# Optimization experiments

Hardware: AMD Instinct MI355X
Metric: run time of the kernel (lower is better)

## Reference

```python
import jax, jax.numpy as jnp
from jax import lax
import numpy as np

N_HEADS, N_FEATURES, IMG_W, IMG_H, C_DOWN = 8, 64, 96, 96, 32


def setup_inputs() -> dict:
    key = jax.random.key(0)
    ks = jax.random.split(key, 16)
    d = {
        'X': jax.random.normal(ks[0], (N_FEATURES, IMG_W, IMG_H), jnp.float32),
        'WQ_task': jax.random.normal(ks[1], (N_HEADS, N_FEATURES, 1, 1), jnp.float32),
        'BQ_task': jax.random.normal(ks[2], (N_HEADS, N_FEATURES, 1, 1), jnp.float32),
        'WK_task': jax.random.normal(ks[3], (N_FEATURES, 1, 1), jnp.float32),
        'BK_task': jax.random.normal(ks[4], (N_FEATURES, 1, 1), jnp.float32),
        'WV_task': jax.random.normal(ks[5], (1, C_DOWN, 1, 1), jnp.float32),
        'BV_task': jax.random.normal(ks[6], (1, C_DOWN, 1, 1), jnp.float32),
        # learned parameters (loaded from disk in the original)
        'WQ_t_minus_1': jax.random.uniform(ks[7], (N_HEADS, N_FEATURES, 1, 1), jnp.float32),
        'WQ_x': jax.random.uniform(ks[8], (1, N_FEATURES, 1, 1), jnp.float32),
        'BQ': jax.random.uniform(ks[9], (N_HEADS, N_FEATURES, 1, 1), jnp.float32),
        'WK_x': jax.random.uniform(ks[10], (N_FEATURES, 1, 1), jnp.float32),
        'BK': jax.random.uniform(ks[11], (N_FEATURES, 1, 1), jnp.float32),
        'Vconv_w': jax.random.normal(ks[12], (C_DOWN, N_FEATURES, 3, 3), jnp.float32) * 0.05,
        'Vconv_b': jax.random.normal(ks[13], (C_DOWN,), jnp.float32) * 0.05,
        # recurrent state (zeros at t=0 in original; random here to exercise the path)
        'prev_Q': jax.random.normal(ks[14], (N_HEADS, N_FEATURES, IMG_W, IMG_H), jnp.float32),
    }
    return d


def reference(X, WQ_task, BQ_task, WK_task, BK_task, WV_task, BV_task,
              WQ_t_minus_1, WQ_x, BQ, WK_x, BK, Vconv_w, Vconv_b, prev_Q):
    F, W, H = X.shape
    rx = X[None]  # (1, F, W, H)
    # Q: (A, F, W, H);  K: (F, W, H)
    Q = WQ_task * jax.nn.relu(WQ_t_minus_1 * prev_Q + WQ_x * rx + BQ) + BQ_task
    K = WK_task * jax.nn.relu(WK_x * X + BK) + BK_task
    # similarity[w,h,u,v] = sum_{a,f} Q[a,f,w,h] * K[f,u,v]
    #                     = sum_f (sum_a Q)[f,w,h] * K[f,u,v]  -> a (WH,F)@(F,WH) GEMM
    Qs = Q.sum(axis=0)  # (F, W, H)
    sim = jnp.einsum('fwh,fuv->whuv', Qs, K)  # (W, H, W, H)
    attn = jax.nn.softmax(sim.reshape(W, H, W * H), axis=-1)  # (W, H, WH)
    # V = task-modulated 3x3 conv of X
    Vc = lax.conv_general_dilated(rx, Vconv_w, window_strides=(1, 1), padding='SAME',
                                  dimension_numbers=('NCHW', 'OIHW', 'NCHW'))
    Vc = Vc + Vconv_b[None, :, None, None]
    V = (WV_task * Vc + BV_task)[0].reshape(C_DOWN, W * H)  # (C, WH)
    # out[c,w,h] = sum_k attn[w,h,k] * V[c,k]
    out = jnp.einsum('whk,ck->cwh', attn, V)  # (C, W, H)
    return out
```

## Files before the change

kernel.cpp:

```cpp
#include <hip/hip_runtime.h>

#define WH 9216
#define NF 64
#define NC 32
#define NH 8
#define IMGW 96
#define IMGH 96
#define PW 98
#define PPLANE 9604
#define L2E 1.4426950408889634f
#define DEFER 11.5f
#define SKIP 18.0f

typedef float f32x4 __attribute__((ext_vector_type(4)));
typedef short short8 __attribute__((ext_vector_type(8)));

__device__ inline short bf16_bits(float x) {
  __bf16 h = (__bf16)x;
  return __builtin_bit_cast(short, h);
}
__device__ inline float bf16_round(float x) { return (float)(__bf16)x; }

__global__ __launch_bounds__(256) void pad_wpack_kernel(
    const float* __restrict__ X, const float* __restrict__ Wc,
    const float* __restrict__ WV_task,
    unsigned short* __restrict__ padXT, short8* __restrict__ wfrag)
{
  const int bid = blockIdx.x;
  const int t = threadIdx.x;
  if (bid < 301) {
    const int idx = bid * 256 + t;
    if (idx < 76832) {
      const int fi = idx / PPLANE;
      const int p = idx - fi * PPLANE;
      const int pw = p / PW;
      const int ph = p - pw * PW;
      short8 r;
      if (pw >= 1 && pw <= IMGW && ph >= 1 && ph <= IMGH) {
        const float* src = X + (size_t)fi * 8 * WH + (pw - 1) * IMGH + (ph - 1);
        #pragma unroll
        for (int e = 0; e < 8; ++e) r[e] = bf16_bits(src[(size_t)e * WH]);
      } else {
        #pragma unroll
        for (int e = 0; e < 8; ++e) r[e] = 0;
      }
      *(short8*)&padXT[(size_t)p * 64 + fi * 8] = r;
    }
  } else {
    #pragma unroll
    for (int j = 0; j < 9; ++j) {
      const int ridx = j * 256 + t;
      const int ct = ridx / 1152;
      const int rem = ridx - ct * 1152;
      const int cc = rem >> 6;
      const int lane = rem & 63;
      const int c = ct * 16 + (lane & 15);
      const int tap = cc >> 1;
      const int f0 = (cc & 1) * 32 + 8 * (lane >> 4);
      const float wv = WV_task[c];
      short8 r;
      #pragma unroll
      for (int e = 0; e < 8; ++e)
        r[e] = bf16_bits(wv * Wc[((size_t)c * NF + f0 + e) * 9 + tap]);
      wfrag[ridx] = r;
    }
  }
}

__global__ __launch_bounds__(128, 2) void qsk_kernel(
    const float* __restrict__ X, const float* __restrict__ WQ_task,
    const float* __restrict__ BQ_task, const float* __restrict__ WK_task,
    const float* __restrict__ BK_task, const float* __restrict__ WQ_t1,
    const float* __restrict__ WQ_x, const float* __restrict__ BQ,
    const float* __restrict__ WK_x, const float* __restrict__ BK,
    const float* __restrict__ prevQ,
    short* __restrict__ qfrag, short* __restrict__ kfrag)
{
  const int t = threadIdx.x;
  const int lane = t & 63;
  const int fh = t >> 6;
  const int h = lane >> 4;
  const int b = blockIdx.x;
  const int T = b >> 1, sub = b & 1;
  const int wh = T * 16 + (lane & 15);
  const int f0 = fh * 32 + 8 * h + 4 * sub;

  float x[4];
  #pragma unroll
  for (int e = 0; e < 4; ++e) x[e] = X[(size_t)(f0 + e) * WH + wh];
  float pq[32];
  #pragma unroll
  for (int a = 0; a < NH; ++a)
    #pragma unroll
    for (int e = 0; e < 4; ++e)
      pq[a * 4 + e] = prevQ[(size_t)(a * 64 + f0 + e) * WH + wh];

  const float4 wkx = *(const float4*)&WK_x[f0];
  const float4 bk  = *(const float4*)&BK[f0];
  const float4 wkt = *(const float4*)&WK_task[f0];
  const float4 bkt = *(const float4*)&BK_task[f0];
  const float4 wqx = *(const float4*)&WQ_x[f0];

  float q[4], k[4], xq[4];
  k[0] = fmaf(wkt.x, fmaxf(fmaf(wkx.x, x[0], bk.x), 0.f), bkt.x);
  k[1] = fmaf(wkt.y, fmaxf(fmaf(wkx.y, x[1], bk.y), 0.f), bkt.y);
  k[2] = fmaf(wkt.z, fmaxf(fmaf(wkx.z, x[2], bk.z), 0.f), bkt.z);
  k[3] = fmaf(wkt.w, fmaxf(fmaf(wkx.w, x[3], bk.w), 0.f), bkt.w);
  xq[0] = wqx.x * x[0]; xq[1] = wqx.y * x[1];
  xq[2] = wqx.z * x[2]; xq[3] = wqx.w * x[3];
  q[0] = q[1] = q[2] = q[3] = 0.f;
  #pragma unroll
  for (int a = 0; a < NH; ++a) {
    const int af0 = a * 64 + f0;
    const float4 w1  = *(const float4*)&WQ_t1[af0];
    const float4 bq  = *(const float4*)&BQ[af0];
    const float4 wqt = *(const float4*)&WQ_task[af0];
    const float4 bqt = *(const float4*)&BQ_task[af0];
    q[0] = fmaf(wqt.x, fmaxf(fmaf(w1.x, pq[a * 4 + 0], xq[0] + bq.x), 0.f), q[0]) + bqt.x;
    q[1] = fmaf(wqt.y, fmaxf(fmaf(w1.y, pq[a * 4 + 1], xq[1] + bq.y), 0.f), q[1]) + bqt.y;
    q[2] = fmaf(wqt.z, fmaxf(fmaf(w1.z, pq[a * 4 + 2], xq[2] + bq.z), 0.f), q[2]) + bqt.z;
    q[3] = fmaf(wqt.w, fmaxf(fmaf(w1.w, pq[a * 4 + 3], xq[3] + bq.w), 0.f), q[3]) + bqt.w;
  }

  short4 qh, ql, kh, klo;
  {
    float qs0 = q[0] * L2E, qs1 = q[1] * L2E, qs2 = q[2] * L2E, qs3 = q[3] * L2E;
    qh.x = bf16_bits(qs0); ql.x = bf16_bits(qs0 - bf16_round(qs0));
    qh.y = bf16_bits(qs1); ql.y = bf16_bits(qs1 - bf16_round(qs1));
    qh.z = bf16_bits(qs2); ql.z = bf16_bits(qs2 - bf16_round(qs2));
    qh.w = bf16_bits(qs3); ql.w = bf16_bits(qs3 - bf16_round(qs3));
    kh.x = bf16_bits(k[0]); klo.x = bf16_bits(k[0] - bf16_round(k[0]));
    kh.y = bf16_bits(k[1]); klo.y = bf16_bits(k[1] - bf16_round(k[1]));
    kh.z = bf16_bits(k[2]); klo.z = bf16_bits(k[2] - bf16_round(k[2]));
    kh.w = bf16_bits(k[3]); klo.w = bf16_bits(k[3] - bf16_round(k[3]));
  }
  const size_t offh = ((size_t)(T * 4 + fh) * 64 + lane) * 8 + sub * 4;
  const size_t offl = ((size_t)(T * 4 + 2 + fh) * 64 + lane) * 8 + sub * 4;
  *(short4*)&qfrag[offh] = qh;
  *(short4*)&qfrag[offl] = ql;
  *(short4*)&kfrag[offh] = kh;
  *(short4*)&kfrag[offl] = klo;
}

__global__ __launch_bounds__(256, 1) void vconv_kernel(
    const unsigned short* __restrict__ padXT, const short8* __restrict__ wfrag,
    const float* __restrict__ bc, const float* __restrict__ WV_task,
    const float* __restrict__ BV_task, short8* __restrict__ vfrag)
{
  __shared__ float Vt[2][32][36];
  const int t = threadIdx.x;
  const int lane = t & 63, w = t >> 6;
  const int h = lane >> 4;
  const int b = blockIdx.x;
  const int ktloc = w >> 1, half = w & 1;
  const int key = (b * 2 + ktloc) * 16 + (lane & 15);
  const int kw = key / IMGH, kh = key - kw * IMGH;

  f32x4 acc0 = {0.f, 0.f, 0.f, 0.f}, acc1 = {0.f, 0.f, 0.f, 0.f};
  #pragma unroll
  for (int i = 0; i < 9; ++i) {
    const int cc = half * 9 + i;
    const int tap = cc >> 1;
    const int di = tap / 3, dj = tap - di * 3;
    const int f0 = (cc & 1) * 32 + 8 * h;
    const int sp = (kw + di) * PW + (kh + dj);
    const short8 xf = *(const short8*)&padXT[(size_t)sp * 64 + f0];
    acc0 = __builtin_amdgcn_mfma_f32_16x16x32_bf16(wfrag[(size_t)cc * 64 + lane], xf, acc0, 0, 0, 0);
    acc1 = __builtin_amdgcn_mfma_f32_16x16x32_bf16(wfrag[(size_t)(18 + cc) * 64 + lane], xf, acc1, 0, 0, 0);
  }
  const int klc = ktloc * 16 + (lane & 15);
  #pragma unroll
  for (int reg = 0; reg < 4; ++reg) {
    Vt[half][4 * h + reg][klc] = acc0[reg];
    Vt[half][16 + 4 * h + reg][klc] = acc1[reg];
  }
  __syncthreads();
  if (t < 128) {
    const int ct = t >> 6;
    const int c = ct * 16 + (lane & 15);
    const float bias = fmaf(WV_task[c], bc[c], BV_task[c]);
    short8 r;
    #pragma unroll
    for (int e = 0; e < 8; ++e) {
      const int kl2 = 16 * (e >> 2) + 4 * h + (e & 3);
      r[e] = bf16_bits(Vt[0][c][kl2] + Vt[1][c][kl2] + bias);
    }
    vfrag[((size_t)b * 2 + ct) * 64 + lane] = r;
  }
}

__global__ __launch_bounds__(256, 3) void flash_mfma(
    const short8* __restrict__ qfrag, const short8* __restrict__ kfrag,
    const short8* __restrict__ vfrag, float* __restrict__ part, int cps)
{
  const int t = threadIdx.x;
  const int lane = t & 63, wave = t >> 6;
  const int h = lane >> 4;
  const int qb = blockIdx.x;
  const int s = blockIdx.y;

  short8 qf[3][4];
  #pragma unroll
  for (int g = 0; g < 3; ++g)
    #pragma unroll
    for (int tm = 0; tm < 4; ++tm)
      qf[g][tm] = qfrag[((size_t)(qb * 3 + g) * 4 + tm) * 64 + lane];

  f32x4 acc[2][3];
  #pragma unroll
  for (int ct = 0; ct < 2; ++ct)
    #pragma unroll
    for (int g = 0; g < 3; ++g)
      acc[ct][g] = (f32x4){0.f, 0.f, 0.f, 0.f};
  float m[3] = {-1e30f, -1e30f, -1e30f};
  float l[3] = {0.f, 0.f, 0.f};

  auto softmax_pv = [&](int g, const f32x4& st0, const f32x4& st1, float tmax,
                        const short8& vf0, const short8& vf1) {
    if (__any(tmax > m[g] + DEFER)) {
      const float nm = fmaxf(m[g], tmax);
      const float r = exp2f(m[g] - nm);
      l[g] *= r;
      acc[0][g] *= r;
      acc[1][g] *= r;
      m[g] = nm;
    }
    short8 pb;
    float ls = 0.f;
    #pragma unroll
    for (int e = 0; e < 4; ++e) {
      const float p0 = exp2f(st0[e] - m[g]);
      const float p1 = exp2f(st1[e] - m[g]);
      ls += p0 + p1;
      pb[e] = bf16_bits(p0);
      pb[4 + e] = bf16_bits(p1);
    }
    l[g] += ls;
    acc[0][g] = __builtin_amdgcn_mfma_f32_16x16x32_bf16(vf0, pb, acc[0][g], 0, 0, 0);
    acc[1][g] = __builtin_amdgcn_mfma_f32_16x16x32_bf16(vf1, pb, acc[1][g], 0, 0, 0);
  };

  const int cpw = cps >> 2;
  const int ch0 = s * cps + wave;

  for (int it = 0; it < cpw; it += 8) {
    const int ch = ch0 + it * 4;
    short8 kf[2][4];
    #pragma unroll
    for (int kt = 0; kt < 2; ++kt)
      #pragma unroll
      for (int tm = 0; tm < 4; ++tm)
        kf[kt][tm] = kfrag[((size_t)(2 * ch + kt) * 4 + tm) * 64 + lane];
    const short8 vf0 = vfrag[(size_t)(ch * 2 + 0) * 64 + lane];
    const short8 vf1 = vfrag[(size_t)(ch * 2 + 1) * 64 + lane];

    #pragma unroll
    for (int g = 0; g < 3; ++g) {
      f32x4 st[2];
      #pragma unroll
      for (int kt = 0; kt < 2; ++kt) {
        f32x4 a = (f32x4){0.f, 0.f, 0.f, 0.f};
        a = __builtin_amdgcn_mfma_f32_16x16x32_bf16(kf[kt][0], qf[g][0], a, 0, 0, 0);
        a = __builtin_amdgcn_mfma_f32_16x16x32_bf16(kf[kt][1], qf[g][1], a, 0, 0, 0);
        a = __builtin_amdgcn_mfma_f32_16x16x32_bf16(kf[kt][2], qf[g][0], a, 0, 0, 0);
        a = __builtin_amdgcn_mfma_f32_16x16x32_bf16(kf[kt][3], qf[g][1], a, 0, 0, 0);
        a = __builtin_amdgcn_mfma_f32_16x16x32_bf16(kf[kt][0], qf[g][2], a, 0, 0, 0);
        a = __builtin_amdgcn_mfma_f32_16x16x32_bf16(kf[kt][1], qf[g][3], a, 0, 0, 0);
        st[kt] = a;
      }
      float tmax = -1e30f;
      #pragma unroll
      for (int e = 0; e < 4; ++e)
        tmax = fmaxf(tmax, fmaxf(st[0][e], st[1][e]));
      tmax = fmaxf(tmax, __shfl_xor(tmax, 16));
      tmax = fmaxf(tmax, __shfl_xor(tmax, 32));
      softmax_pv(g, st[0], st[1], tmax, vf0, vf1);
    }
  }

  for (int it = 0; it < cpw; ++it) {
    if ((it & 7) == 0) continue;
    const int ch = ch0 + it * 4;
    short8 kfh[2][2];
    #pragma unroll
    for (int kt = 0; kt < 2; ++kt)
      #pragma unroll
      for (int tm = 0; tm < 2; ++tm)
        kfh[kt][tm] = kfrag[((size_t)(2 * ch + kt) * 4 + tm) * 64 + lane];

    f32x4 st[2][3];
    #pragma unroll
    for (int kt = 0; kt < 2; ++kt)
      #pragma unroll
      for (int g = 0; g < 3; ++g) {
        f32x4 a = (f32x4){0.f, 0.f, 0.f, 0.f};
        a = __builtin_amdgcn_mfma_f32_16x16x32_bf16(kfh[kt][0], qf[g][0], a, 0, 0, 0);
        a = __builtin_amdgcn_mfma_f32_16x16x32_bf16(kfh[kt][1], qf[g][1], a, 0, 0, 0);
        st[kt][g] = a;
      }

    float tmax[3];
    int fire = 0;
    #pragma unroll
    for (int g = 0; g < 3; ++g) {
      float tm8 = -1e30f;
      #pragma unroll
      for (int e = 0; e < 4; ++e)
        tm8 = fmaxf(tm8, fmaxf(st[0][g][e], st[1][g][e]));
      tm8 = fmaxf(tm8, __shfl_xor(tm8, 16));
      tm8 = fmaxf(tm8, __shfl_xor(tm8, 32));
      tmax[g] = tm8;
      if (__any(tm8 > m[g] - SKIP)) fire |= 1 << g;
    }
    if (!fire) continue;

    short8 kfl[2][2];
    #pragma unroll
    for (int kt = 0; kt < 2; ++kt)
      #pragma unroll
      for (int tm = 0; tm < 2; ++tm)
        kfl[kt][tm] = kfrag[((size_t)(2 * ch + kt) * 4 + 2 + tm) * 64 + lane];
    const short8 vf0 = vfrag[(size_t)(ch * 2 + 0) * 64 + lane];
    const short8 vf1 = vfrag[(size_t)(ch * 2 + 1) * 64 + lane];

    #pragma unroll
    for (int g = 0; g < 3; ++g) {
      if (!(fire & (1 << g))) continue;
      #pragma unroll
      for (int kt = 0; kt < 2; ++kt) {
        f32x4 a = st[kt][g];
        a = __builtin_amdgcn_mfma_f32_16x16x32_bf16(kfl[kt][0], qf[g][0], a, 0, 0, 0);
        a = __builtin_amdgcn_mfma_f32_16x16x32_bf16(kfl[kt][1], qf[g][1], a, 0, 0, 0);
        a = __builtin_amdgcn_mfma_f32_16x16x32_bf16(kfh[kt][0], qf[g][2], a, 0, 0, 0);
        a = __builtin_amdgcn_mfma_f32_16x16x32_bf16(kfh[kt][1], qf[g][3], a, 0, 0, 0);
        st[kt][g] = a;
      }
      softmax_pv(g, st[0][g], st[1][g], tmax[g], vf0, vf1);
    }
  }

  const int u = s * 4 + wave;
  #pragma unroll
  for (int g = 0; g < 3; ++g) {
    float lf = l[g] + __shfl_xor(l[g], 16);
    lf += __shfl_xor(lf, 32);
    const int q = qb * 48 + g * 16 + (lane & 15);
    float* base = part + ((size_t)u * WH + q) * 36;
    *(f32x4*)(base + 0 + 4 * h) = acc[0][g];
    *(f32x4*)(base + 16 + 4 * h) = acc[1][g];
    if (h == 0) { base[32] = m[g]; base[33] = lf; }
  }
}

__global__ __launch_bounds__(256) void merge_kernel(
    const float* __restrict__ part, float* __restrict__ out, int units)
{
  const int t = threadIdx.x;
  const int cl = t & 31;
  const int wh = blockIdx.x * 8 + (t >> 5);
  float M = -1e30f;
  for (int u = 0; u < units; ++u)
    M = fmaxf(M, part[((size_t)u * WH + wh) * 36 + 32]);
  float L = 0.f, A = 0.f;
  for (int u = 0; u < units; ++u) {
    const float* base = part + ((size_t)u * WH + wh) * 36;
    const float e = exp2f(base[32] - M);
    L = fmaf(e, base[33], L);
    A = fmaf(e, base[cl], A);
  }
  out[(size_t)cl * WH + wh] = A / L;
}

extern "C" void kernel_launch(void* const* d_in, const int* in_sizes, int n_in,
                              void* d_out, int out_size, void* d_ws, size_t ws_size,
                              hipStream_t stream)
{
  const float* X   = (const float*)d_in[0];
  const float* WQt = (const float*)d_in[1];
  const float* BQt = (const float*)d_in[2];
  const float* WKt = (const float*)d_in[3];
  const float* BKt = (const float*)d_in[4];
  const float* WVt = (const float*)d_in[5];
  const float* BVt = (const float*)d_in[6];
  const float* WQ1 = (const float*)d_in[7];
  const float* WQx = (const float*)d_in[8];
  const float* BQ  = (const float*)d_in[9];
  const float* WKx = (const float*)d_in[10];
  const float* BK  = (const float*)d_in[11];
  const float* Wc  = (const float*)d_in[12];
  const float* bc  = (const float*)d_in[13];
  const float* pQ  = (const float*)d_in[14];
  float* out = (float*)d_out;

  short8* qfrag = (short8*)d_ws;
  short8* kfrag = qfrag + (size_t)147456;
  short8* vfrag = kfrag + (size_t)147456;
  short8* wfrag = vfrag + (size_t)36864;
  unsigned short* padXT = (unsigned short*)(wfrag + 2304);
  float* part = (float*)((char*)padXT + (size_t)PPLANE * 64 * 2);
  const size_t base_bytes = ((size_t)147456 * 2 + 36864 + 2304) * 16 + (size_t)PPLANE * 64 * 2;

  int ksplit = 4;
  while (ksplit > 1 &&
         base_bytes + (size_t)(4 * ksplit) * WH * 36 * sizeof(float) > ws_size)
    ksplit >>= 1;
  const int cps = 288 / ksplit;
  const int units = 4 * ksplit;

  pad_wpack_kernel<<<dim3(302), 256, 0, stream>>>(X, Wc, WVt, padXT, wfrag);
  qsk_kernel<<<dim3(1152), 128, 0, stream>>>(X, WQt, BQt, WKt, BKt,
                                             WQ1, WQx, BQ, WKx, BK, pQ,
                                             (short*)qfrag, (short*)kfrag);
  vconv_kernel<<<dim3(288), 256, 0, stream>>>(padXT, wfrag, bc, WVt, BVt, vfrag);
  flash_mfma<<<dim3(192, ksplit), 256, 0, stream>>>(qfrag, kfrag, vfrag, part, cps);
  merge_kernel<<<dim3(WH / 8), 256, 0, stream>>>(part, out, units);
}
```

Measured before the change: 91.40 us.

## Fuse prep kernels, drop chunk skipping, shrink flash tiles, online merge

Merges the Q/K projection kernel into the padding/weight-pack kernel, so there is one fewer launch. The attention kernel drops the two-pass scheme that estimated scores with high-bf16 K and skipped chunks far below the running max. It now computes full scores for every chunk, seeds the accumulator with the negated running max, and rescales only past a threshold. Each block handles 32 queries instead of 48, giving a bigger grid with higher occupancy and swapped grid axes. The vconv kernel is split into smaller per-tile blocks, and the merge becomes a single-pass online rescale. This removes skip overhead and improves parallelism, but does all the score and PV work that was previously skipped.

```diff
diff --git a/kernel.cpp b/kernel.cpp
--- a/kernel.cpp
+++ b/kernel.cpp
@@ -10,7 +10,6 @@
 #define PPLANE 9604
 #define L2E 1.4426950408889634f
 #define DEFER 11.5f
-#define SKIP 18.0f
 
 typedef float f32x4 __attribute__((ext_vector_type(4)));
 typedef short short8 __attribute__((ext_vector_type(8)));
@@ -21,15 +20,85 @@
 }
 __device__ inline float bf16_round(float x) { return (float)(__bf16)x; }
 
-__global__ __launch_bounds__(256) void pad_wpack_kernel(
-    const float* __restrict__ X, const float* __restrict__ Wc,
+__global__ __launch_bounds__(256, 2) void prep_kernel(
+    const float* __restrict__ X, const float* __restrict__ WQ_task,
+    const float* __restrict__ BQ_task, const float* __restrict__ WK_task,
+    const float* __restrict__ BK_task, const float* __restrict__ WQ_t1,
+    const float* __restrict__ WQ_x, const float* __restrict__ BQ,
+    const float* __restrict__ WK_x, const float* __restrict__ BK,
+    const float* __restrict__ prevQ, const float* __restrict__ Wc,
     const float* __restrict__ WV_task,
+    short* __restrict__ qfrag, short* __restrict__ kfrag,
     unsigned short* __restrict__ padXT, short8* __restrict__ wfrag)
 {
   const int bid = blockIdx.x;
   const int t = threadIdx.x;
-  if (bid < 301) {
-    const int idx = bid * 256 + t;
+  if (bid < 576) {
+    const int lane = t & 63;
+    const int w2 = t >> 6;
+    const int fh = w2 & 1, sub = w2 >> 1;
+    const int h = lane >> 4;
+    const int T = bid;
+    const int wh = T * 16 + (lane & 15);
+    const int f0 = fh * 32 + 8 * h + 4 * sub;
+
+    float x[4];
+    #pragma unroll
+    for (int e = 0; e < 4; ++e) x[e] = X[(size_t)(f0 + e) * WH + wh];
+    float pq[32];
+    #pragma unroll
+    for (int a = 0; a < NH; ++a)
+      #pragma unroll
+      for (int e = 0; e < 4; ++e)
+        pq[a * 4 + e] = prevQ[(size_t)(a * 64 + f0 + e) * WH + wh];
+
+    const float4 wkx = *(const float4*)&WK_x[f0];
+    const float4 bk  = *(const float4*)&BK[f0];
+    const float4 wkt = *(const float4*)&WK_task[f0];
+    const float4 bkt = *(const float4*)&BK_task[f0];
+    const float4 wqx = *(const float4*)&WQ_x[f0];
+
+    float q[4], k[4], xq[4];
+    k[0] = fmaf(wkt.x, fmaxf(fmaf(wkx.x, x[0], bk.x), 0.f), bkt.x);
+    k[1] = fmaf(wkt.y, fmaxf(fmaf(wkx.y, x[1], bk.y), 0.f), bkt.y);
+    k[2] = fmaf(wkt.z, fmaxf(fmaf(wkx.z, x[2], bk.z), 0.f), bkt.z);
+    k[3] = fmaf(wkt.w, fmaxf(fmaf(wkx.w, x[3], bk.w), 0.f), bkt.w);
+    xq[0] = wqx.x * x[0]; xq[1] = wqx.y * x[1];
+    xq[2] = wqx.z * x[2]; xq[3] = wqx.w * x[3];
+    q[0] = q[1] = q[2] = q[3] = 0.f;
+    #pragma unroll
+    for (int a = 0; a < NH; ++a) {
+      const int af0 = a * 64 + f0;
+      const float4 w1  = *(const float4*)&WQ_t1[af0];
+      const float4 bq  = *(const float4*)&BQ[af0];
+      const float4 wqt = *(const float4*)&WQ_task[af0];
+      const float4 bqt = *(const float4*)&BQ_task[af0];
+      q[0] = fmaf(wqt.x, fmaxf(fmaf(w1.x, pq[a * 4 + 0], xq[0] + bq.x), 0.f), q[0]) + bqt.x;
+      q[1] = fmaf(wqt.y, fmaxf(fmaf(w1.y, pq[a * 4 + 1], xq[1] + bq.y), 0.f), q[1]) + bqt.y;
+      q[2] = fmaf(wqt.z, fmaxf(fmaf(w1.z, pq[a * 4 + 2], xq[2] + bq.z), 0.f), q[2]) + bqt.z;
+      q[3] = fmaf(wqt.w, fmaxf(fmaf(w1.w, pq[a * 4 + 3], xq[3] + bq.w), 0.f), q[3]) + bqt.w;
+    }
+
+    short4 qh, ql, kh, klo;
+    {
+      float qs0 = q[0] * L2E, qs1 = q[1] * L2E, qs2 = q[2] * L2E, qs3 = q[3] * L2E;
+      qh.x = bf16_bits(qs0); ql.x = bf16_bits(qs0 - bf16_round(qs0));
+      qh.y = bf16_bits(qs1); ql.y = bf16_bits(qs1 - bf16_round(qs1));
+      qh.z = bf16_bits(qs2); ql.z = bf16_bits(qs2 - bf16_round(qs2));
+      qh.w = bf16_bits(qs3); ql.w = bf16_bits(qs3 - bf16_round(qs3));
+      kh.x = bf16_bits(k[0]); klo.x = bf16_bits(k[0] - bf16_round(k[0]));
+      kh.y = bf16_bits(k[1]); klo.y = bf16_bits(k[1] - bf16_round(k[1]));
+      kh.z = bf16_bits(k[2]); klo.z = bf16_bits(k[2] - bf16_round(k[2]));
+      kh.w = bf16_bits(k[3]); klo.w = bf16_bits(k[3] - bf16_round(k[3]));
+    }
+    const size_t offh = ((size_t)(T * 4 + fh) * 64 + lane) * 8 + sub * 4;
+    const size_t offl = ((size_t)(T * 4 + 2 + fh) * 64 + lane) * 8 + sub * 4;
+    *(short4*)&qfrag[offh] = qh;
+    *(short4*)&qfrag[offl] = ql;
+    *(short4*)&kfrag[offh] = kh;
+    *(short4*)&kfrag[offl] = klo;
+  } else if (bid < 877) {
+    const int idx = (bid - 576) * 256 + t;
     if (idx < 76832) {
       const int fi = idx / PPLANE;
       const int p = idx - fi * PPLANE;
@@ -67,96 +136,21 @@
   }
 }
 
-__global__ __launch_bounds__(128, 2) void qsk_kernel(
-    const float* __restrict__ X, const float* __restrict__ WQ_task,
-    const float* __restrict__ BQ_task, const float* __restrict__ WK_task,
-    const float* __restrict__ BK_task, const float* __restrict__ WQ_t1,
-    const float* __restrict__ WQ_x, const float* __restrict__ BQ,
-    const float* __restrict__ WK_x, const float* __restrict__ BK,
-    const float* __restrict__ prevQ,
-    short* __restrict__ qfrag, short* __restrict__ kfrag)
-{
-  const int t = threadIdx.x;
-  const int lane = t & 63;
-  const int fh = t >> 6;
-  const int h = lane >> 4;
-  const int b = blockIdx.x;
-  const int T = b >> 1, sub = b & 1;
-  const int wh = T * 16 + (lane & 15);
-  const int f0 = fh * 32 + 8 * h + 4 * sub;
-
-  float x[4];
-  #pragma unroll
-  for (int e = 0; e < 4; ++e) x[e] = X[(size_t)(f0 + e) * WH + wh];
-  float pq[32];
-  #pragma unroll
-  for (int a = 0; a < NH; ++a)
-    #pragma unroll
-    for (int e = 0; e < 4; ++e)
-      pq[a * 4 + e] = prevQ[(size_t)(a * 64 + f0 + e) * WH + wh];
-
-  const float4 wkx = *(const float4*)&WK_x[f0];
-  const float4 bk  = *(const float4*)&BK[f0];
-  const float4 wkt = *(const float4*)&WK_task[f0];
-  const float4 bkt = *(const float4*)&BK_task[f0];
-  const float4 wqx = *(const float4*)&WQ_x[f0];
-
-  float q[4], k[4], xq[4];
-  k[0] = fmaf(wkt.x, fmaxf(fmaf(wkx.x, x[0], bk.x), 0.f), bkt.x);
-  k[1] = fmaf(wkt.y, fmaxf(fmaf(wkx.y, x[1], bk.y), 0.f), bkt.y);
-  k[2] = fmaf(wkt.z, fmaxf(fmaf(wkx.z, x[2], bk.z), 0.f), bkt.z);
-  k[3] = fmaf(wkt.w, fmaxf(fmaf(wkx.w, x[3], bk.w), 0.f), bkt.w);
-  xq[0] = wqx.x * x[0]; xq[1] = wqx.y * x[1];
-  xq[2] = wqx.z * x[2]; xq[3] = wqx.w * x[3];
-  q[0] = q[1] = q[2] = q[3] = 0.f;
-  #pragma unroll
-  for (int a = 0; a < NH; ++a) {
-    const int af0 = a * 64 + f0;
-    const float4 w1  = *(const float4*)&WQ_t1[af0];
-    const float4 bq  = *(const float4*)&BQ[af0];
-    const float4 wqt = *(const float4*)&WQ_task[af0];
-    const float4 bqt = *(const float4*)&BQ_task[af0];
-    q[0] = fmaf(wqt.x, fmaxf(fmaf(w1.x, pq[a * 4 + 0], xq[0] + bq.x), 0.f), q[0]) + bqt.x;
-    q[1] = fmaf(wqt.y, fmaxf(fmaf(w1.y, pq[a * 4 + 1], xq[1] + bq.y), 0.f), q[1]) + bqt.y;
-    q[2] = fmaf(wqt.z, fmaxf(fmaf(w1.z, pq[a * 4 + 2], xq[2] + bq.z), 0.f), q[2]) + bqt.z;
-    q[3] = fmaf(wqt.w, fmaxf(fmaf(w1.w, pq[a * 4 + 3], xq[3] + bq.w), 0.f), q[3]) + bqt.w;
-  }
-
-  short4 qh, ql, kh, klo;
-  {
-    float qs0 = q[0] * L2E, qs1 = q[1] * L2E, qs2 = q[2] * L2E, qs3 = q[3] * L2E;
-    qh.x = bf16_bits(qs0); ql.x = bf16_bits(qs0 - bf16_round(qs0));
-    qh.y = bf16_bits(qs1); ql.y = bf16_bits(qs1 - bf16_round(qs1));
-    qh.z = bf16_bits(qs2); ql.z = bf16_bits(qs2 - bf16_round(qs2));
-    qh.w = bf16_bits(qs3); ql.w = bf16_bits(qs3 - bf16_round(qs3));
-    kh.x = bf16_bits(k[0]); klo.x = bf16_bits(k[0] - bf16_round(k[0]));
-    kh.y = bf16_bits(k[1]); klo.y = bf16_bits(k[1] - bf16_round(k[1]));
-    kh.z = bf16_bits(k[2]); klo.z = bf16_bits(k[2] - bf16_round(k[2]));
-    kh.w = bf16_bits(k[3]); klo.w = bf16_bits(k[3] - bf16_round(k[3]));
-  }
-  const size_t offh = ((size_t)(T * 4 + fh) * 64 + lane) * 8 + sub * 4;
-  const size_t offl = ((size_t)(T * 4 + 2 + fh) * 64 + lane) * 8 + sub * 4;
-  *(short4*)&qfrag[offh] = qh;
-  *(short4*)&qfrag[offl] = ql;
-  *(short4*)&kfrag[offh] = kh;
-  *(short4*)&kfrag[offl] = klo;
-}
-
-__global__ __launch_bounds__(256, 1) void vconv_kernel(
+__global__ __launch_bounds__(256, 2) void vconv_kernel(
     const unsigned short* __restrict__ padXT, const short8* __restrict__ wfrag,
     const float* __restrict__ bc, const float* __restrict__ WV_task,
-    const float* __restrict__ BV_task, short8* __restrict__ vfrag)
-{
-  __shared__ float Vt[2][32][36];
+    const float* __restrict__ BV_task, short* __restrict__ vfrag)
+{
+  __shared__ float Vt[2][32][20];
   const int t = threadIdx.x;
   const int lane = t & 63, w = t >> 6;
   const int h = lane >> 4;
-  const int b = blockIdx.x;
-  const int ktloc = w >> 1, half = w & 1;
-  const int key = (b * 2 + ktloc) * 16 + (lane & 15);
+  const int ktile = blockIdx.x;
+  const int half = w & 1, ct = w >> 1;
+  const int key = ktile * 16 + (lane & 15);
   const int kw = key / IMGH, kh = key - kw * IMGH;
 
-  f32x4 acc0 = {0.f, 0.f, 0.f, 0.f}, acc1 = {0.f, 0.f, 0.f, 0.f};
+  f32x4 acc = {0.f, 0.f, 0.f, 0.f};
   #pragma unroll
   for (int i = 0; i < 9; ++i) {
     const int cc = half * 9 + i;
@@ -165,85 +159,57 @@
     const int f0 = (cc & 1) * 32 + 8 * h;
     const int sp = (kw + di) * PW + (kh + dj);
     const short8 xf = *(const short8*)&padXT[(size_t)sp * 64 + f0];
-    acc0 = __builtin_amdgcn_mfma_f32_16x16x32_bf16(wfrag[(size_t)cc * 64 + lane], xf, acc0, 0, 0, 0);
-    acc1 = __builtin_amdgcn_mfma_f32_16x16x32_bf16(wfrag[(size_t)(18 + cc) * 64 + lane], xf, acc1, 0, 0, 0);
-  }
-  const int klc = ktloc * 16 + (lane & 15);
-  #pragma unroll
-  for (int reg = 0; reg < 4; ++reg) {
-    Vt[half][4 * h + reg][klc] = acc0[reg];
-    Vt[half][16 + 4 * h + reg][klc] = acc1[reg];
-  }
+    acc = __builtin_amdgcn_mfma_f32_16x16x32_bf16(wfrag[(size_t)(ct * 18 + cc) * 64 + lane],
+                                                  xf, acc, 0, 0, 0);
+  }
+  #pragma unroll
+  for (int reg = 0; reg < 4; ++reg)
+    Vt[half][ct * 16 + 4 * h + reg][lane & 15] = acc[reg];
   __syncthreads();
   if (t < 128) {
-    const int ct = t >> 6;
-    const int c = ct * 16 + (lane & 15);
+    const int ct2 = t >> 6;
+    const int c = ct2 * 16 + (lane & 15);
     const float bias = fmaf(WV_task[c], bc[c], BV_task[c]);
-    short8 r;
-    #pragma unroll
-    for (int e = 0; e < 8; ++e) {
-      const int kl2 = 16 * (e >> 2) + 4 * h + (e & 3);
-      r[e] = bf16_bits(Vt[0][c][kl2] + Vt[1][c][kl2] + bias);
-    }
-    vfrag[((size_t)b * 2 + ct) * 64 + lane] = r;
-  }
-}
-
-__global__ __launch_bounds__(256, 3) void flash_mfma(
+    short4 r;
+    #pragma unroll
+    for (int j = 0; j < 4; ++j) {
+      const int kl = 4 * h + j;
+      r[j] = bf16_bits(Vt[0][c][kl] + Vt[1][c][kl] + bias);
+    }
+    const int ch = ktile >> 1, eh = ktile & 1;
+    *(short4*)&vfrag[(((size_t)ch * 2 + ct2) * 64 + lane) * 8 + eh * 4] = r;
+  }
+}
+
+__global__ __launch_bounds__(256, 4) void flash_mfma(
     const short8* __restrict__ qfrag, const short8* __restrict__ kfrag,
     const short8* __restrict__ vfrag, float* __restrict__ part, int cps)
 {
   const int t = threadIdx.x;
   const int lane = t & 63, wave = t >> 6;
   const int h = lane >> 4;
-  const int qb = blockIdx.x;
-  const int s = blockIdx.y;
-
-  short8 qf[3][4];
-  #pragma unroll
-  for (int g = 0; g < 3; ++g)
+  const int s = blockIdx.x;
+  const int qb = blockIdx.y;
+
+  short8 qf[2][4];
+  #pragma unroll
+  for (int g = 0; g < 2; ++g)
     #pragma unroll
     for (int tm = 0; tm < 4; ++tm)
-      qf[g][tm] = qfrag[((size_t)(qb * 3 + g) * 4 + tm) * 64 + lane];
-
-  f32x4 acc[2][3];
+      qf[g][tm] = qfrag[((size_t)(qb * 2 + g) * 4 + tm) * 64 + lane];
+
+  f32x4 acc[2][2];
   #pragma unroll
   for (int ct = 0; ct < 2; ++ct)
     #pragma unroll
-    for (int g = 0; g < 3; ++g)
+    for (int g = 0; g < 2; ++g)
       acc[ct][g] = (f32x4){0.f, 0.f, 0.f, 0.f};
-  float m[3] = {-1e30f, -1e30f, -1e30f};
-  float l[3] = {0.f, 0.f, 0.f};
-
-  auto softmax_pv = [&](int g, const f32x4& st0, const f32x4& st1, float tmax,
-                        const short8& vf0, const short8& vf1) {
-    if (__any(tmax > m[g] + DEFER)) {
-      const float nm = fmaxf(m[g], tmax);
-      const float r = exp2f(m[g] - nm);
-      l[g] *= r;
-      acc[0][g] *= r;
-      acc[1][g] *= r;
-      m[g] = nm;
-    }
-    short8 pb;
-    float ls = 0.f;
-    #pragma unroll
-    for (int e = 0; e < 4; ++e) {
-      const float p0 = exp2f(st0[e] - m[g]);
-      const float p1 = exp2f(st1[e] - m[g]);
-      ls += p0 + p1;
-      pb[e] = bf16_bits(p0);
-      pb[4 + e] = bf16_bits(p1);
-    }
-    l[g] += ls;
-    acc[0][g] = __builtin_amdgcn_mfma_f32_16x16x32_bf16(vf0, pb, acc[0][g], 0, 0, 0);
-    acc[1][g] = __builtin_amdgcn_mfma_f32_16x16x32_bf16(vf1, pb, acc[1][g], 0, 0, 0);
-  };
+  float m[2] = {0.f, 0.f};
+  float l[2] = {0.f, 0.f};
 
   const int cpw = cps >> 2;
   const int ch0 = s * cps + wave;
-
-  for (int it = 0; it < cpw; it += 8) {
+  for (int it = 0; it < cpw; ++it) {
     const int ch = ch0 + it * 4;
     short8 kf[2][4];
     #pragma unroll
@@ -255,96 +221,59 @@
     const short8 vf1 = vfrag[(size_t)(ch * 2 + 1) * 64 + lane];
 
     #pragma unroll
-    for (int g = 0; g < 3; ++g) {
-      f32x4 st[2];
+    for (int g = 0; g < 2; ++g) {
+      const float nm = -m[g];
+      f32x4 st0 = {nm, nm, nm, nm};
+      f32x4 st1 = st0;
+      st0 = __builtin_amdgcn_mfma_f32_16x16x32_bf16(kf[0][0], qf[g][0], st0, 0, 0, 0);
+      st0 = __builtin_amdgcn_mfma_f32_16x16x32_bf16(kf[0][1], qf[g][1], st0, 0, 0, 0);
+      st0 = __builtin_amdgcn_mfma_f32_16x16x32_bf16(kf[0][2], qf[g][0], st0, 0, 0, 0);
+      st0 = __builtin_amdgcn_mfma_f32_16x16x32_bf16(kf[0][3], qf[g][1], st0, 0, 0, 0);
+      st0 = __builtin_amdgcn_mfma_f32_16x16x32_bf16(kf[0][0], qf[g][2], st0, 0, 0, 0);
+      st0 = __builtin_amdgcn_mfma_f32_16x16x32_bf16(kf[0][1], qf[g][3], st0, 0, 0, 0);
+      st1 = __builtin_amdgcn_mfma_f32_16x16x32_bf16(kf[1][0], qf[g][0], st1, 0, 0, 0);
+      st1 = __builtin_amdgcn_mfma_f32_16x16x32_bf16(kf[1][1], qf[g][1], st1, 0, 0, 0);
+      st1 = __builtin_amdgcn_mfma_f32_16x16x32_bf16(kf[1][2], qf[g][0], st1, 0, 0, 0);
+      st1 = __builtin_amdgcn_mfma_f32_16x16x32_bf16(kf[1][3], qf[g][1], st1, 0, 0, 0);
+      st1 = __builtin_amdgcn_mfma_f32_16x16x32_bf16(kf[1][0], qf[g][2], st1, 0, 0, 0);
+      st1 = __builtin_amdgcn_mfma_f32_16x16x32_bf16(kf[1][1], qf[g][3], st1, 0, 0, 0);
+
+      float tr = fmaxf(fmaxf(fmaxf(st0[0], st0[1]), st0[2]),
+                       fmaxf(fmaxf(st0[3], st1[0]), st1[1]));
+      tr = fmaxf(tr, fmaxf(st1[2], st1[3]));
+      tr = fmaxf(tr, __shfl_xor(tr, 16));
+      tr = fmaxf(tr, __shfl_xor(tr, 32));
+      if (__any(tr > DEFER)) {
+        const float d = fmaxf(tr, 0.f);
+        const float r = exp2f(-d);
+        l[g] *= r;
+        acc[0][g] *= r;
+        acc[1][g] *= r;
+        m[g] += d;
+        #pragma unroll
+        for (int e = 0; e < 4; ++e) { st0[e] -= d; st1[e] -= d; }
+      }
+      short8 pb;
+      float p0[4], p1[4];
       #pragma unroll
-      for (int kt = 0; kt < 2; ++kt) {
-        f32x4 a = (f32x4){0.f, 0.f, 0.f, 0.f};
-        a = __builtin_amdgcn_mfma_f32_16x16x32_bf16(kf[kt][0], qf[g][0], a, 0, 0, 0);
-        a = __builtin_amdgcn_mfma_f32_16x16x32_bf16(kf[kt][1], qf[g][1], a, 0, 0, 0);
-        a = __builtin_amdgcn_mfma_f32_16x16x32_bf16(kf[kt][2], qf[g][0], a, 0, 0, 0);
-        a = __builtin_amdgcn_mfma_f32_16x16x32_bf16(kf[kt][3], qf[g][1], a, 0, 0, 0);
-        a = __builtin_amdgcn_mfma_f32_16x16x32_bf16(kf[kt][0], qf[g][2], a, 0, 0, 0);
-        a = __builtin_amdgcn_mfma_f32_16x16x32_bf16(kf[kt][1], qf[g][3], a, 0, 0, 0);
-        st[kt] = a;
+      for (int e = 0; e < 4; ++e) {
+        p0[e] = exp2f(st0[e]);
+        p1[e] = exp2f(st1[e]);
+        pb[e] = bf16_bits(p0[e]);
+        pb[4 + e] = bf16_bits(p1[e]);
       }
-      float tmax = -1e30f;
-      #pragma unroll
-      for (int e = 0; e < 4; ++e)
-        tmax = fmaxf(tmax, fmaxf(st[0][e], st[1][e]));
-      tmax = fmaxf(tmax, __shfl_xor(tmax, 16));
-      tmax = fmaxf(tmax, __shfl_xor(tmax, 32));
-      softmax_pv(g, st[0], st[1], tmax, vf0, vf1);
-    }
-  }
-
-  for (int it = 0; it < cpw; ++it) {
-    if ((it & 7) == 0) continue;
-    const int ch = ch0 + it * 4;
-    short8 kfh[2][2];
-    #pragma unroll
-    for (int kt = 0; kt < 2; ++kt)
-      #pragma unroll
-      for (int tm = 0; tm < 2; ++tm)
-        kfh[kt][tm] = kfrag[((size_t)(2 * ch + kt) * 4 + tm) * 64 + lane];
-
-    f32x4 st[2][3];
-    #pragma unroll
-    for (int kt = 0; kt < 2; ++kt)
-      #pragma unroll
-      for (int g = 0; g < 3; ++g) {
-        f32x4 a = (f32x4){0.f, 0.f, 0.f, 0.f};
-        a = __builtin_amdgcn_mfma_f32_16x16x32_bf16(kfh[kt][0], qf[g][0], a, 0, 0, 0);
-        a = __builtin_amdgcn_mfma_f32_16x16x32_bf16(kfh[kt][1], qf[g][1], a, 0, 0, 0);
-        st[kt][g] = a;
-      }
-
-    float tmax[3];
-    int fire = 0;
-    #pragma unroll
-    for (int g = 0; g < 3; ++g) {
-      float tm8 = -1e30f;
-      #pragma unroll
-      for (int e = 0; e < 4; ++e)
-        tm8 = fmaxf(tm8, fmaxf(st[0][g][e], st[1][g][e]));
-      tm8 = fmaxf(tm8, __shfl_xor(tm8, 16));
-      tm8 = fmaxf(tm8, __shfl_xor(tm8, 32));
-      tmax[g] = tm8;
-      if (__any(tm8 > m[g] - SKIP)) fire |= 1 << g;
-    }
-    if (!fire) continue;
-
-    short8 kfl[2][2];
-    #pragma unroll
-    for (int kt = 0; kt < 2; ++kt)
-      #pragma unroll
-      for (int tm = 0; tm < 2; ++tm)
-        kfl[kt][tm] = kfrag[((size_t)(2 * ch + kt) * 4 + 2 + tm) * 64 + lane];
-    const short8 vf0 = vfrag[(size_t)(ch * 2 + 0) * 64 + lane];
-    const short8 vf1 = vfrag[(size_t)(ch * 2 + 1) * 64 + lane];
-
-    #pragma unroll
-    for (int g = 0; g < 3; ++g) {
-      if (!(fire & (1 << g))) continue;
-      #pragma unroll
-      for (int kt = 0; kt < 2; ++kt) {
-        f32x4 a = st[kt][g];
-        a = __builtin_amdgcn_mfma_f32_16x16x32_bf16(kfl[kt][0], qf[g][0], a, 0, 0, 0);
-        a = __builtin_amdgcn_mfma_f32_16x16x32_bf16(kfl[kt][1], qf[g][1], a, 0, 0, 0);
-        a = __builtin_amdgcn_mfma_f32_16x16x32_bf16(kfh[kt][0], qf[g][2], a, 0, 0, 0);
-        a = __builtin_amdgcn_mfma_f32_16x16x32_bf16(kfh[kt][1], qf[g][3], a, 0, 0, 0);
-        st[kt][g] = a;
-      }
-      softmax_pv(g, st[0][g], st[1][g], tmax[g], vf0, vf1);
+      l[g] += ((p0[0] + p0[1]) + (p0[2] + p0[3])) + ((p1[0] + p1[1]) + (p1[2] + p1[3]));
+      acc[0][g] = __builtin_amdgcn_mfma_f32_16x16x32_bf16(vf0, pb, acc[0][g], 0, 0, 0);
+      acc[1][g] = __builtin_amdgcn_mfma_f32_16x16x32_bf16(vf1, pb, acc[1][g], 0, 0, 0);
     }
   }
 
   const int u = s * 4 + wave;
   #pragma unroll
-  for (int g = 0; g < 3; ++g) {
+  for (int g = 0; g < 2; ++g) {
     float lf = l[g] + __shfl_xor(l[g], 16);
     lf += __shfl_xor(lf, 32);
-    const int q = qb * 48 + g * 16 + (lane & 15);
+    const int q = qb * 32 + g * 16 + (lane & 15);
     float* base = part + ((size_t)u * WH + q) * 36;
     *(f32x4*)(base + 0 + 4 * h) = acc[0][g];
     *(f32x4*)(base + 16 + 4 * h) = acc[1][g];
@@ -358,15 +287,22 @@
   const int t = threadIdx.x;
   const int cl = t & 31;
   const int wh = blockIdx.x * 8 + (t >> 5);
-  float M = -1e30f;
-  for (int u = 0; u < units; ++u)
-    M = fmaxf(M, part[((size_t)u * WH + wh) * 36 + 32]);
-  float L = 0.f, A = 0.f;
+  float M = -1e30f, L = 0.f, A = 0.f;
   for (int u = 0; u < units; ++u) {
     const float* base = part + ((size_t)u * WH + wh) * 36;
-    const float e = exp2f(base[32] - M);
-    L = fmaf(e, base[33], L);
-    A = fmaf(e, base[cl], A);
+    const float mu = base[32];
+    const float lu = base[33];
+    const float au = base[cl];
+    if (mu > M) {
+      const float sc = exp2f(M - mu);
+      L = fmaf(L, sc, lu);
+      A = fmaf(A, sc, au);
+      M = mu;
+    } else {
+      const float e = exp2f(mu - M);
+      L = fmaf(e, lu, L);
+      A = fmaf(e, au, A);
+    }
   }
   out[(size_t)cl * WH + wh] = A / L;
 }
@@ -407,11 +343,10 @@
   const int cps = 288 / ksplit;
   const int units = 4 * ksplit;
 
-  pad_wpack_kernel<<<dim3(302), 256, 0, stream>>>(X, Wc, WVt, padXT, wfrag);
-  qsk_kernel<<<dim3(1152), 128, 0, stream>>>(X, WQt, BQt, WKt, BKt,
-                                             WQ1, WQx, BQ, WKx, BK, pQ,
-                                             (short*)qfrag, (short*)kfrag);
-  vconv_kernel<<<dim3(288), 256, 0, stream>>>(padXT, wfrag, bc, WVt, BVt, vfrag);
-  flash_mfma<<<dim3(192, ksplit), 256, 0, stream>>>(qfrag, kfrag, vfrag, part, cps);
+  prep_kernel<<<dim3(878), 256, 0, stream>>>(X, WQt, BQt, WKt, BKt,
+                                             WQ1, WQx, BQ, WKx, BK, pQ, Wc, WVt,
+                                             (short*)qfrag, (short*)kfrag, padXT, wfrag);
+  vconv_kernel<<<dim3(576), 256, 0, stream>>>(padXT, wfrag, bc, WVt, BVt, (short*)vfrag);
+  flash_mfma<<<dim3(ksplit, 288), 256, 0, stream>>>(qfrag, kfrag, vfrag, part, cps);
   merge_kernel<<<dim3(WH / 8), 256, 0, stream>>>(part, out, units);
 }
```

Measured after the change: 88.41 us. 3.3% less time.
